# Kernel tuning notes

Hardware: AMD Instinct MI355X
Metric: run time of the kernel (lower is better)

## Reference

```python
import jax, jax.numpy as jnp
import numpy as np

N, E = 50000, 1600000
F_IN, C1, H, C2, G, NCLS = 256, 16, 4, 32, 64, 10


def setup_inputs() -> dict:
    ks = jax.random.split(jax.random.key(0), 14)
    x = jax.random.normal(ks[0], (N, F_IN), dtype=jnp.float32)
    edge_index = jax.random.randint(ks[1], (2, E), 0, N, dtype=jnp.int32)
    batch = jnp.sort(jax.random.randint(ks[2], (N,), 0, G, dtype=jnp.int32))
    s1 = 1.0 / np.sqrt(F_IN)
    s2 = 1.0 / np.sqrt(H * C1)
    s3 = 1.0 / np.sqrt(C2)
    return {
        "x": x,
        "edge_index": edge_index,
        "batch": batch,
        "W1": jax.random.normal(ks[3], (F_IN, H * C1), jnp.float32) * s1,
        "att_src1": jax.random.normal(ks[4], (H, C1), jnp.float32) * s2,
        "att_dst1": jax.random.normal(ks[5], (H, C1), jnp.float32) * s2,
        "b1": jnp.zeros((H * C1,), jnp.float32),
        "W2": jax.random.normal(ks[6], (H * C1, C2), jnp.float32) * s2,
        "att_src2": jax.random.normal(ks[7], (1, C2), jnp.float32) * s3,
        "att_dst2": jax.random.normal(ks[8], (1, C2), jnp.float32) * s3,
        "b2": jnp.zeros((C2,), jnp.float32),
        "fc_w": jax.random.normal(ks[9], (C2, NCLS), jnp.float32) * s3,
        "fc_b": jnp.zeros((NCLS,), jnp.float32),
    }


def _gat_conv(x, src, dst, W, a_src, a_dst, b, concat):
    # PyG GATConv: linear per head, LeakyReLU(0.2) edge scores,
    # softmax over incoming edges per destination node, weighted scatter-sum.
    n = x.shape[0]
    heads, ch = a_src.shape
    h = (x @ W).reshape(n, heads, ch)                       # [N, H, C]
    a_s = (h * a_src).sum(-1)                               # [N, H]
    a_d = (h * a_dst).sum(-1)                               # [N, H]
    e = jax.nn.leaky_relu(a_s[src] + a_d[dst], 0.2)         # [E', H]
    m = jax.ops.segment_max(e, dst, num_segments=n)         # [N, H]
    w = jnp.exp(e - m[dst])
    den = jax.ops.segment_sum(w, dst, num_segments=n)
    alpha = w / den[dst]                                    # [E', H]
    out = jax.ops.segment_sum(alpha[:, :, None] * h[src], dst, num_segments=n)
    out = out.reshape(n, heads * ch) if concat else out.mean(axis=1)
    return out + b


def reference(x, edge_index, batch, W1, att_src1, att_dst1, b1,
              W2, att_src2, att_dst2, b2, fc_w, fc_b):
    n = x.shape[0]
    loops = jnp.arange(n, dtype=edge_index.dtype)           # add_self_loops=True
    src = jnp.concatenate([edge_index[0], loops])
    dst = jnp.concatenate([edge_index[1], loops])

    h = jax.nn.elu(_gat_conv(x, src, dst, W1, att_src1, att_dst1, b1, True))
    h = jax.nn.elu(_gat_conv(h, src, dst, W2, att_src2, att_dst2, b2, False))

    # global mean pool over graphs
    sums = jax.ops.segment_sum(h, batch, num_segments=G)    # [G, C2]
    cnt = jax.ops.segment_sum(jnp.ones((n,), h.dtype), batch, num_segments=G)
    pooled = sums / jnp.maximum(cnt, 1.0)[:, None]

    logits = pooled @ fc_w + fc_b
    return jax.nn.log_softmax(logits, axis=1)
```

## Files before the change

### kernel.cpp

```cpp
#include <hip/hip_runtime.h>
#include <hip/hip_bf16.h>

#define GV 64
#define NCLSV 10
#define C2V 32

using short8 = __attribute__((ext_vector_type(8))) short;
using short4v = __attribute__((ext_vector_type(4))) short;
using f32x4 = __attribute__((ext_vector_type(4))) float;

__device__ __forceinline__ float lrelu(float v) { return v > 0.f ? v : 0.2f * v; }
__device__ __forceinline__ float eluf(float v) { return v > 0.f ? v : expf(v) - 1.f; }

__device__ __forceinline__ unsigned short fbf(float f) {
    unsigned u = __float_as_uint(f);
    u += 0x7fff + ((u >> 16) & 1);
    return (unsigned short)(u >> 16);
}
__device__ __forceinline__ float bff(unsigned short h) {
    return __uint_as_float((unsigned)h << 16);
}
__device__ __forceinline__ unsigned f2h(float f) {
    union { _Float16 h; unsigned short u; } cv;
    cv.h = (_Float16)f;
    return (unsigned)cv.u;
}
__device__ __forceinline__ float h2f(unsigned short u) {
    union { unsigned short u; _Float16 h; } cv;
    cv.u = u;
    return (float)cv.h;
}

__global__ void zero_kernel(int* p, int n) {
    int i = blockIdx.x * blockDim.x + threadIdx.x;
    if (i < n) p[i] = 0;
}

__global__ void wprep_kernel(const float* __restrict__ W1, const float* __restrict__ W2,
                             short* __restrict__ wt, short* __restrict__ wt2) {
    int t = blockIdx.x * blockDim.x + threadIdx.x;
    for (int e = t; e < 16384; e += gridDim.x * blockDim.x) {
        int k = e >> 6, ch = e & 63;
        wt[ch * 256 + k] = (short)fbf(W1[e]);
    }
    for (int e = t; e < 2048; e += gridDim.x * blockDim.x) {
        int k = e >> 5, ch = e & 31;
        wt2[ch * 64 + k] = (short)fbf(W2[e]);
    }
}

__global__ __launch_bounds__(256) void gemm1_mfma_kernel(
    const float* __restrict__ x, const short* __restrict__ wt,
    const float* __restrict__ as_w, const float* __restrict__ ad_w,
    unsigned short* __restrict__ h1b, float* __restrict__ as1, float* __restrict__ ad1, int N) {
    __shared__ __align__(16) short xs[32 * 256];
    int b0 = blockIdx.x * 32;
    int tid = threadIdx.x;
    #pragma unroll
    for (int i = 0; i < 8; ++i) {
        int e = (tid + i * 256) * 4;
        int node = e >> 8, k = e & 255;
        float4 v = make_float4(0.f, 0.f, 0.f, 0.f);
        if (b0 + node < N) v = *(const float4*)&x[(size_t)(b0 + node) * 256 + k];
        short4v hv;
        hv[0] = (short)fbf(v.x); hv[1] = (short)fbf(v.y);
        hv[2] = (short)fbf(v.z); hv[3] = (short)fbf(v.w);
        int bo = node * 512 + k * 2;
        int sw = bo ^ ((node & 7) << 4);
        *(short4v*)((char*)xs + sw) = hv;
    }
    __syncthreads();
    int w = tid >> 6, lane = tid & 63;
    int ng = w >> 1, cg = w & 1;
    int g = lane >> 4, q = lane & 15;
    int rowb = ng * 16 + q;
    int kb = g * 8;
    f32x4 acc[2];
    acc[0] = (f32x4){0.f, 0.f, 0.f, 0.f};
    acc[1] = (f32x4){0.f, 0.f, 0.f, 0.f};
    #pragma unroll
    for (int ks = 0; ks < 8; ++ks) {
        int kk = ks * 32 + kb;
        int off = (rowb * 512 + kk * 2) ^ ((rowb & 7) << 4);
        short8 a = *(const short8*)((const char*)xs + off);
        #pragma unroll
        for (int ct = 0; ct < 2; ++ct) {
            int ch = cg * 32 + ct * 16 + q;
            short8 b = *(const short8*)(wt + ch * 256 + kk);
            acc[ct] = __builtin_amdgcn_mfma_f32_16x16x32_bf16(a, b, acc[ct], 0, 0, 0);
        }
    }
    #pragma unroll
    for (int ct = 0; ct < 2; ++ct) {
        int chi = cg * 32 + ct * 16 + q;
        float asw = as_w[chi], adw = ad_w[chi];
        int head = cg * 2 + ct;
        #pragma unroll
        for (int r = 0; r < 4; ++r) {
            int node = b0 + ng * 16 + g * 4 + r;
            float val = acc[ct][r];
            if (node < N) h1b[(size_t)node * 64 + chi] = fbf(val);
            float vs = val * asw, vd = val * adw;
            vs += __shfl_xor(vs, 1); vs += __shfl_xor(vs, 2);
            vs += __shfl_xor(vs, 4); vs += __shfl_xor(vs, 8);
            vd += __shfl_xor(vd, 1); vd += __shfl_xor(vd, 2);
            vd += __shfl_xor(vd, 4); vd += __shfl_xor(vd, 8);
            if (q == 0 && node < N) {
                as1[node * 4 + head] = vs;
                ad1[node * 4 + head] = vd;
            }
        }
    }
}

__global__ __launch_bounds__(256) void bucketPre_kernel(
    const int* __restrict__ ei, int E, int EE, int* __restrict__ bcnt,
    int* __restrict__ pbase) {
    __shared__ int hist[256];
    int span = (EE + gridDim.x - 1) / gridDim.x;
    int s0 = blockIdx.x * span;
    int s1 = min(s0 + span, EE);
    hist[threadIdx.x] = 0;
    __syncthreads();
    for (int i = s0 + threadIdx.x; i < s1; i += 256) {
        int d = (i < E) ? ei[E + i] : i - E;
        atomicAdd(&hist[d >> 8], 1);
    }
    __syncthreads();
    int c = hist[threadIdx.x];
    int base = 0;
    if (c) base = atomicAdd(&bcnt[threadIdx.x], c);
    pbase[blockIdx.x * 256 + threadIdx.x] = base;
}

__global__ void bscan_kernel(const int* __restrict__ bcnt, int* __restrict__ bucketoff,
                             int* __restrict__ rowoff, int N, int EE) {
    __shared__ int wtot[4];
    int v = bcnt[threadIdx.x];
    int lane = threadIdx.x & 63, w = threadIdx.x >> 6;
    int inc = v;
    for (int o = 1; o < 64; o <<= 1) { int t = __shfl_up(inc, o); if (lane >= o) inc += t; }
    if (lane == 63) wtot[w] = inc;
    __syncthreads();
    int woff = 0;
    #pragma unroll
    for (int i = 0; i < 4; ++i) woff += (i < w) ? wtot[i] : 0;
    bucketoff[threadIdx.x + 1] = woff + inc;
    if (threadIdx.x == 0) { bucketoff[0] = 0; rowoff[N] = EE; }
}

__global__ __launch_bounds__(256) void bucketA_kernel(
    const int* __restrict__ ei, int E, int EE,
    const int* __restrict__ bucketoff, const int* __restrict__ pbase,
    int* __restrict__ bbuf) {
    __shared__ int base[256];
    __shared__ int cur[256];
    int span = (EE + gridDim.x - 1) / gridDim.x;
    int s0 = blockIdx.x * span;
    int s1 = min(s0 + span, EE);
    if (s0 >= s1) return;
    base[threadIdx.x] = bucketoff[threadIdx.x] + pbase[blockIdx.x * 256 + threadIdx.x];
    cur[threadIdx.x] = 0;
    __syncthreads();
    for (int i = s0 + threadIdx.x; i < s1; i += 256) {
        int s, d;
        if (i < E) { s = ei[i]; d = ei[E + i]; } else { s = d = i - E; }
        int b = d >> 8;
        int lr = atomicAdd(&cur[b], 1);
        bbuf[base[b] + lr] = ((d & 255) << 24) | s;
    }
}

__global__ __launch_bounds__(256) void bucketB_kernel(
    const int* __restrict__ bucketoff, const int* __restrict__ bbuf,
    const float* __restrict__ as1, const float* __restrict__ ad1,
    int* __restrict__ rowoff, int* __restrict__ ssrc, int4* __restrict__ wrec, int N) {
    int k = blockIdx.x;
    __shared__ int cnt[256];
    __shared__ int excl[256];
    __shared__ int cur[256];
    __shared__ int wtot[4];
    cnt[threadIdx.x] = 0; cur[threadIdx.x] = 0;
    __syncthreads();
    int lo = bucketoff[k], hi = bucketoff[k + 1];
    for (int i = lo + threadIdx.x; i < hi; i += 256)
        atomicAdd(&cnt[(bbuf[i] >> 24) & 255], 1);
    __syncthreads();
    int v = cnt[threadIdx.x];
    int lane = threadIdx.x & 63, w = threadIdx.x >> 6;
    int inc = v;
    for (int o = 1; o < 64; o <<= 1) { int t = __shfl_up(inc, o); if (lane >= o) inc += t; }
    if (lane == 63) wtot[w] = inc;
    __syncthreads();
    int woff = 0;
    #pragma unroll
    for (int i = 0; i < 4; ++i) woff += (i < w) ? wtot[i] : 0;
    int e = woff + inc - v;
    excl[threadIdx.x] = e;
    int dst = (k << 8) + threadIdx.x;
    if (dst < N) rowoff[dst] = lo + e;
    __syncthreads();
    int dbase = k << 8;
    for (int i = lo + threadIdx.x; i < hi; i += 256) {
        int pv = bbuf[i];
        int dlow = (pv >> 24) & 255;
        int s = pv & 0xFFFFFF;
        int d = dbase + dlow;
        int lr = atomicAdd(&cur[dlow], 1);
        int pos = lo + excl[dlow] + lr;
        ssrc[pos] = s;
        float4 a4 = *(const float4*)&as1[s * 4];
        float4 d4 = *(const float4*)&ad1[d * 4];
        float w0 = __expf(lrelu(a4.x + d4.x));
        float w1 = __expf(lrelu(a4.y + d4.y));
        float w2 = __expf(lrelu(a4.z + d4.z));
        float w3 = __expf(lrelu(a4.w + d4.w));
        int4 rec;
        rec.x = s;
        rec.y = (int)(f2h(w0) | (f2h(w1) << 16));
        rec.z = (int)(f2h(w2) | (f2h(w3) << 16));
        rec.w = 0;
        wrec[pos] = rec;
    }
}

__global__ __launch_bounds__(256) void gat1_kernel(
    const int* __restrict__ rowoff, const int4* __restrict__ wrec,
    const unsigned short* __restrict__ h1b, const float* __restrict__ b1,
    unsigned short* __restrict__ h2b, int N) {
    int wv = threadIdx.x >> 6;
    int lane = threadIdx.x & 63;
    int row = blockIdx.x * 4 + wv;
    if (row >= N) return;
    int beg = rowoff[row], end = rowoff[row + 1];
    int par = lane >> 3, co = lane & 7, hq = co >> 1;
    float den = 0.f;
    float a[8];
    #pragma unroll
    for (int i = 0; i < 8; ++i) a[i] = 0.f;
    for (int t = beg + par; t < end; t += 8) {
        int4 rec = wrec[t];
        unsigned wpair = (hq & 2) ? (unsigned)rec.z : (unsigned)rec.y;
        unsigned wb = (hq & 1) ? (wpair >> 16) : (wpair & 0xFFFFu);
        float w = h2f((unsigned short)wb);
        den += w;
        short8 p = *(const short8*)&h1b[(size_t)rec.x * 64 + 8 * co];
        a[0] += w * bff((unsigned short)p[0]);
        a[1] += w * bff((unsigned short)p[1]);
        a[2] += w * bff((unsigned short)p[2]);
        a[3] += w * bff((unsigned short)p[3]);
        a[4] += w * bff((unsigned short)p[4]);
        a[5] += w * bff((unsigned short)p[5]);
        a[6] += w * bff((unsigned short)p[6]);
        a[7] += w * bff((unsigned short)p[7]);
    }
    den += __shfl_xor(den, 8);
    den += __shfl_xor(den, 16);
    den += __shfl_xor(den, 32);
    #pragma unroll
    for (int i = 0; i < 8; ++i) {
        a[i] += __shfl_xor(a[i], 8);
        a[i] += __shfl_xor(a[i], 16);
        a[i] += __shfl_xor(a[i], 32);
    }
    if (par == 0) {
        float r = 1.f / den;
        short8 o;
        #pragma unroll
        for (int i = 0; i < 8; ++i)
            o[i] = (short)fbf(eluf(a[i] * r + b1[8 * co + i]));
        *(short8*)&h2b[(size_t)row * 64 + 8 * co] = o;
    }
}

__global__ __launch_bounds__(256) void gemm2_mfma_kernel(
    const unsigned short* __restrict__ h2b, const short* __restrict__ wt2,
    const float* __restrict__ as_w, const float* __restrict__ ad_w,
    unsigned short* __restrict__ t2b, float* __restrict__ as2, float* __restrict__ ad2, int N) {
    __shared__ __align__(16) short xs[64 * 64];
    int b0 = blockIdx.x * 64;
    int tid = threadIdx.x;
    #pragma unroll
    for (int i = 0; i < 2; ++i) {
        int e = (tid + i * 256) * 8;
        int node = e >> 6, k = e & 63;
        short8 v = (short8){0, 0, 0, 0, 0, 0, 0, 0};
        if (b0 + node < N) v = *(const short8*)&h2b[(size_t)(b0 + node) * 64 + k];
        int bo = node * 128 + k * 2;
        int sw = bo ^ ((node & 7) << 4);
        *(short8*)((char*)xs + sw) = v;
    }
    __syncthreads();
    int w = tid >> 6, lane = tid & 63;
    int g = lane >> 4, q = lane & 15;
    int rowb = w * 16 + q;
    int kb = g * 8;
    f32x4 acc[2];
    acc[0] = (f32x4){0.f, 0.f, 0.f, 0.f};
    acc[1] = (f32x4){0.f, 0.f, 0.f, 0.f};
    #pragma unroll
    for (int ks = 0; ks < 2; ++ks) {
        int kk = ks * 32 + kb;
        int off = (rowb * 128 + kk * 2) ^ ((rowb & 7) << 4);
        short8 a = *(const short8*)((const char*)xs + off);
        #pragma unroll
        for (int ct = 0; ct < 2; ++ct) {
            int ch = ct * 16 + q;
            short8 b = *(const short8*)(wt2 + ch * 64 + kk);
            acc[ct] = __builtin_amdgcn_mfma_f32_16x16x32_bf16(a, b, acc[ct], 0, 0, 0);
        }
    }
    float asw0 = as_w[q], adw0 = ad_w[q];
    float asw1 = as_w[16 + q], adw1 = ad_w[16 + q];
    #pragma unroll
    for (int r = 0; r < 4; ++r) {
        int node = b0 + w * 16 + g * 4 + r;
        float v0 = acc[0][r], v1 = acc[1][r];
        if (node < N) {
            t2b[(size_t)node * 32 + q] = fbf(v0);
            t2b[(size_t)node * 32 + 16 + q] = fbf(v1);
        }
        float vs = v0 * asw0 + v1 * asw1;
        float vd = v0 * adw0 + v1 * adw1;
        vs += __shfl_xor(vs, 1); vs += __shfl_xor(vs, 2);
        vs += __shfl_xor(vs, 4); vs += __shfl_xor(vs, 8);
        vd += __shfl_xor(vd, 1); vd += __shfl_xor(vd, 2);
        vd += __shfl_xor(vd, 4); vd += __shfl_xor(vd, 8);
        if (q == 0 && node < N) {
            as2[node] = vs;
            ad2[node] = vd;
        }
    }
}

__global__ __launch_bounds__(256) void gat2_kernel(
    const int* __restrict__ rowoff, const int* __restrict__ ssrc,
    const float* __restrict__ as2, const float* __restrict__ ad2,
    const unsigned short* __restrict__ t2b, const float* __restrict__ b2,
    float* __restrict__ h3, int N) {
    int wv = threadIdx.x >> 6;
    int lane = threadIdx.x & 63;
    int row = blockIdx.x * 4 + wv;
    if (row >= N) return;
    int beg = rowoff[row], end = rowoff[row + 1];
    int par = lane >> 2, co = lane & 3;
    float adv = ad2[row];
    float den = 0.f;
    float a[8];
    #pragma unroll
    for (int i = 0; i < 8; ++i) a[i] = 0.f;
    for (int t = beg + par; t < end; t += 16) {
        int s0 = ssrc[t];
        float w = __expf(lrelu(as2[s0] + adv));
        den += w;
        short8 p = *(const short8*)&t2b[(size_t)s0 * 32 + 8 * co];
        a[0] += w * bff((unsigned short)p[0]);
        a[1] += w * bff((unsigned short)p[1]);
        a[2] += w * bff((unsigned short)p[2]);
        a[3] += w * bff((unsigned short)p[3]);
        a[4] += w * bff((unsigned short)p[4]);
        a[5] += w * bff((unsigned short)p[5]);
        a[6] += w * bff((unsigned short)p[6]);
        a[7] += w * bff((unsigned short)p[7]);
    }
    den += __shfl_xor(den, 4);
    den += __shfl_xor(den, 8);
    den += __shfl_xor(den, 16);
    den += __shfl_xor(den, 32);
    #pragma unroll
    for (int i = 0; i < 8; ++i) {
        a[i] += __shfl_xor(a[i], 4);
        a[i] += __shfl_xor(a[i], 8);
        a[i] += __shfl_xor(a[i], 16);
        a[i] += __shfl_xor(a[i], 32);
    }
    if (par == 0) {
        float r = 1.f / den;
        float4 o0, o1;
        o0.x = eluf(a[0] * r + b2[8 * co]);
        o0.y = eluf(a[1] * r + b2[8 * co + 1]);
        o0.z = eluf(a[2] * r + b2[8 * co + 2]);
        o0.w = eluf(a[3] * r + b2[8 * co + 3]);
        o1.x = eluf(a[4] * r + b2[8 * co + 4]);
        o1.y = eluf(a[5] * r + b2[8 * co + 5]);
        o1.z = eluf(a[6] * r + b2[8 * co + 6]);
        o1.w = eluf(a[7] * r + b2[8 * co + 7]);
        *(float4*)&h3[(size_t)row * 32 + 8 * co] = o0;
        *(float4*)&h3[(size_t)row * 32 + 8 * co + 4] = o1;
    }
}

__device__ __forceinline__ int lowerb(const int* __restrict__ a, int n, int v) {
    int lo = 0, hi = n;
    while (lo < hi) {
        int mid = (lo + hi) >> 1;
        if (a[mid] < v) lo = mid + 1; else hi = mid;
    }
    return lo;
}

__global__ __launch_bounds__(256) void pool_kernel(
    const float* __restrict__ h3, const int* __restrict__ batch,
    float* __restrict__ pooled, float* __restrict__ cnt, int N) {
    int g = blockIdx.x;
    __shared__ int bounds[2];
    if (threadIdx.x == 0) bounds[0] = lowerb(batch, N, g);
    else if (threadIdx.x == 1) bounds[1] = lowerb(batch, N, g + 1);
    __syncthreads();
    int lo = bounds[0], hi = bounds[1];
    int c = threadIdx.x & 31;
    int grp = threadIdx.x >> 5;
    float s = 0.f;
    for (int n = lo + grp; n < hi; n += 8) s += h3[(size_t)n * 32 + c];
    __shared__ float red[8][33];
    red[grp][c] = s;
    __syncthreads();
    if (grp == 0) {
        float t = 0.f;
        for (int k = 0; k < 8; ++k) t += red[k][c];
        pooled[g * C2V + c] = t;
        if (c == 0) cnt[g] = (float)(hi - lo);
    }
}

__global__ void final_kernel(const float* __restrict__ pooled, const float* __restrict__ cnt,
                             const float* __restrict__ fc_w, const float* __restrict__ fc_b,
                             float* __restrict__ out) {
    int g = threadIdx.x;
    if (g >= GV) return;
    float c = cnt[g];
    c = c > 1.f ? c : 1.f;
    float p[C2V];
    for (int j = 0; j < C2V; ++j) p[j] = pooled[g * C2V + j] / c;
    float l[NCLSV];
    float mx = -1e30f;
    for (int k = 0; k < NCLSV; ++k) {
        float acc = fc_b[k];
        for (int j = 0; j < C2V; ++j) acc += p[j] * fc_w[j * NCLSV + k];
        l[k] = acc;
        mx = fmaxf(mx, acc);
    }
    float s = 0.f;
    for (int k = 0; k < NCLSV; ++k) s += expf(l[k] - mx);
    float lse = mx + logf(s);
    for (int k = 0; k < NCLSV; ++k) out[g * NCLSV + k] = l[k] - lse;
}

extern "C" void kernel_launch(void* const* d_in, const int* in_sizes, int n_in,
                              void* d_out, int out_size, void* d_ws, size_t ws_size,
                              hipStream_t stream) {
    const float* x = (const float*)d_in[0];
    const int* ei = (const int*)d_in[1];
    const int* batch = (const int*)d_in[2];
    const float* W1 = (const float*)d_in[3];
    const float* att_src1 = (const float*)d_in[4];
    const float* att_dst1 = (const float*)d_in[5];
    const float* b1 = (const float*)d_in[6];
    const float* W2 = (const float*)d_in[7];
    const float* att_src2 = (const float*)d_in[8];
    const float* att_dst2 = (const float*)d_in[9];
    const float* b2 = (const float*)d_in[10];
    const float* fc_w = (const float*)d_in[11];
    const float* fc_b = (const float*)d_in[12];
    float* out = (float*)d_out;

    int N = in_sizes[0] / 256;
    int E = in_sizes[1] / 2;
    int EE = E + N;
    int NB = (N + 255) >> 8;

    float* ws = (float*)d_ws;
    size_t off = 0;
    int* bcnt = (int*)(ws + off);      off += 256;
    size_t zTot = off;
    int* pbase = (int*)(ws + off);     off += 1024 * 256;
    int* bucketoff = (int*)(ws + off); off += 257;
    float* pooled = ws + off;          off += (size_t)GV * C2V;
    float* cnt = ws + off;             off += (size_t)GV;
    int* rowoff = (int*)(ws + off);    off += (size_t)N + 1;
    int* bbuf = (int*)(ws + off);      off += (size_t)EE;
    int* ssrc = (int*)(ws + off);      off += (size_t)EE;
    off = (off + 3) & ~(size_t)3;
    int4* wrec = (int4*)(ws + off);    off += (size_t)4 * EE;
    short* wt = (short*)(ws + off);    off += 8192;
    short* wt2 = (short*)(ws + off);   off += 1024;
    unsigned short* h1b = (unsigned short*)(ws + off); off += (size_t)32 * N;
    float* as1 = ws + off;             off += (size_t)4 * N;
    float* ad1 = ws + off;             off += (size_t)4 * N;
    unsigned short* h2b = (unsigned short*)(ws + off); off += (size_t)32 * N;
    unsigned short* t2b = (unsigned short*)(ws + off); off += (size_t)16 * N;
    float* as2 = ws + off;             off += (size_t)N;
    float* ad2 = ws + off;             off += (size_t)N;
    float* h3 = ws + off;              off += (size_t)32 * N;

    zero_kernel<<<1, 256, 0, stream>>>((int*)ws, (int)zTot);
    wprep_kernel<<<9, 256, 0, stream>>>(W1, W2, wt, wt2);

    gemm1_mfma_kernel<<<(N + 31) / 32, 256, 0, stream>>>(
        x, wt, att_src1, att_dst1, h1b, as1, ad1, N);

    bucketPre_kernel<<<1024, 256, 0, stream>>>(ei, E, EE, bcnt, pbase);
    bscan_kernel<<<1, 256, 0, stream>>>(bcnt, bucketoff, rowoff, N, EE);
    bucketA_kernel<<<1024, 256, 0, stream>>>(ei, E, EE, bucketoff, pbase, bbuf);
    bucketB_kernel<<<NB, 256, 0, stream>>>(bucketoff, bbuf, as1, ad1, rowoff, ssrc, wrec, N);

    gat1_kernel<<<(N + 3) / 4, 256, 0, stream>>>(rowoff, wrec, h1b, b1, h2b, N);

    gemm2_mfma_kernel<<<(N + 63) / 64, 256, 0, stream>>>(
        h2b, wt2, att_src2, att_dst2, t2b, as2, ad2, N);

    gat2_kernel<<<(N + 3) / 4, 256, 0, stream>>>(rowoff, ssrc, as2, ad2, t2b, b2, h3, N);

    pool_kernel<<<GV, 256, 0, stream>>>(h3, batch, pooled, cnt, N);
    final_kernel<<<1, 64, 0, stream>>>(pooled, cnt, fc_w, fc_b, out);
}
```

Before: 233.4 us.

## Split layer-1 features into head-pair halves and aggregate in two passes

Layer-1 node features are stored as two 32-channel tables, one per head pair, instead of one 64-channel table. The edge-weight computation moves out of bucketB into a new per-row edgew kernel that writes two 8-byte records per edge. gat1 then runs twice, once per half, with 16 edges in flight per wave. Each pass gathers from a table half the size, aiming for better cache hit rates on the random source gathers. The cost is an extra kernel launch, a second pass over rowoff and the edge records, and duplicated source indices in both record arrays.

New measurement: 249.8 us. 1.07x slower.

```diff
diff --git a/kernel.cpp b/kernel.cpp
--- a/kernel.cpp
+++ b/kernel.cpp
@@ -52,7 +52,8 @@
 __global__ __launch_bounds__(256) void gemm1_mfma_kernel(
     const float* __restrict__ x, const short* __restrict__ wt,
     const float* __restrict__ as_w, const float* __restrict__ ad_w,
-    unsigned short* __restrict__ h1b, float* __restrict__ as1, float* __restrict__ ad1, int N) {
+    unsigned short* __restrict__ h1lo, unsigned short* __restrict__ h1hi,
+    float* __restrict__ as1, float* __restrict__ ad1, int N) {
     __shared__ __align__(16) short xs[32 * 256];
     int b0 = blockIdx.x * 32;
     int tid = threadIdx.x;
@@ -90,16 +91,18 @@
             acc[ct] = __builtin_amdgcn_mfma_f32_16x16x32_bf16(a, b, acc[ct], 0, 0, 0);
         }
     }
+    unsigned short* dst = cg ? h1hi : h1lo;
     #pragma unroll
     for (int ct = 0; ct < 2; ++ct) {
         int chi = cg * 32 + ct * 16 + q;
+        int ch32 = ct * 16 + q;
         float asw = as_w[chi], adw = ad_w[chi];
         int head = cg * 2 + ct;
         #pragma unroll
         for (int r = 0; r < 4; ++r) {
             int node = b0 + ng * 16 + g * 4 + r;
             float val = acc[ct][r];
-            if (node < N) h1b[(size_t)node * 64 + chi] = fbf(val);
+            if (node < N) dst[(size_t)node * 32 + ch32] = fbf(val);
             float vs = val * asw, vd = val * adw;
             vs += __shfl_xor(vs, 1); vs += __shfl_xor(vs, 2);
             vs += __shfl_xor(vs, 4); vs += __shfl_xor(vs, 8);
@@ -173,8 +176,7 @@
 
 __global__ __launch_bounds__(256) void bucketB_kernel(
     const int* __restrict__ bucketoff, const int* __restrict__ bbuf,
-    const float* __restrict__ as1, const float* __restrict__ ad1,
-    int* __restrict__ rowoff, int* __restrict__ ssrc, int4* __restrict__ wrec, int N) {
+    int* __restrict__ rowoff, int* __restrict__ ssrc, int N) {
     int k = blockIdx.x;
     __shared__ int cnt[256];
     __shared__ int excl[256];
@@ -200,51 +202,56 @@
     int dst = (k << 8) + threadIdx.x;
     if (dst < N) rowoff[dst] = lo + e;
     __syncthreads();
-    int dbase = k << 8;
     for (int i = lo + threadIdx.x; i < hi; i += 256) {
         int pv = bbuf[i];
         int dlow = (pv >> 24) & 255;
-        int s = pv & 0xFFFFFF;
-        int d = dbase + dlow;
         int lr = atomicAdd(&cur[dlow], 1);
-        int pos = lo + excl[dlow] + lr;
-        ssrc[pos] = s;
-        float4 a4 = *(const float4*)&as1[s * 4];
-        float4 d4 = *(const float4*)&ad1[d * 4];
-        float w0 = __expf(lrelu(a4.x + d4.x));
-        float w1 = __expf(lrelu(a4.y + d4.y));
-        float w2 = __expf(lrelu(a4.z + d4.z));
-        float w3 = __expf(lrelu(a4.w + d4.w));
-        int4 rec;
-        rec.x = s;
-        rec.y = (int)(f2h(w0) | (f2h(w1) << 16));
-        rec.z = (int)(f2h(w2) | (f2h(w3) << 16));
-        rec.w = 0;
-        wrec[pos] = rec;
-    }
-}
-
-__global__ __launch_bounds__(256) void gat1_kernel(
-    const int* __restrict__ rowoff, const int4* __restrict__ wrec,
-    const unsigned short* __restrict__ h1b, const float* __restrict__ b1,
-    unsigned short* __restrict__ h2b, int N) {
+        ssrc[lo + excl[dlow] + lr] = pv & 0xFFFFFF;
+    }
+}
+
+__global__ __launch_bounds__(256) void edgew_kernel(
+    const int* __restrict__ rowoff, const int* __restrict__ ssrc,
+    const float* __restrict__ as1, const float* __restrict__ ad1,
+    int2* __restrict__ wrecA, int2* __restrict__ wrecB, int N) {
     int wv = threadIdx.x >> 6;
     int lane = threadIdx.x & 63;
     int row = blockIdx.x * 4 + wv;
     if (row >= N) return;
     int beg = rowoff[row], end = rowoff[row + 1];
-    int par = lane >> 3, co = lane & 7, hq = co >> 1;
+    float4 d4 = *(const float4*)&ad1[row * 4];
+    for (int t = beg + lane; t < end; t += 64) {
+        int s = ssrc[t];
+        float4 a4 = *(const float4*)&as1[s * 4];
+        float w0 = __expf(lrelu(a4.x + d4.x));
+        float w1 = __expf(lrelu(a4.y + d4.y));
+        float w2 = __expf(lrelu(a4.z + d4.z));
+        float w3 = __expf(lrelu(a4.w + d4.w));
+        wrecA[t] = make_int2(s, (int)(f2h(w0) | (f2h(w1) << 16)));
+        wrecB[t] = make_int2(s, (int)(f2h(w2) | (f2h(w3) << 16)));
+    }
+}
+
+__global__ __launch_bounds__(256) void gat1_kernel(
+    const int* __restrict__ rowoff, const int2* __restrict__ wrec,
+    const unsigned short* __restrict__ tab, const float* __restrict__ b1,
+    unsigned short* __restrict__ h2b, int N, int ho) {
+    int wv = threadIdx.x >> 6;
+    int lane = threadIdx.x & 63;
+    int row = blockIdx.x * 4 + wv;
+    if (row >= N) return;
+    int beg = rowoff[row], end = rowoff[row + 1];
+    int par = lane >> 2, co = lane & 3;
     float den = 0.f;
     float a[8];
     #pragma unroll
     for (int i = 0; i < 8; ++i) a[i] = 0.f;
-    for (int t = beg + par; t < end; t += 8) {
-        int4 rec = wrec[t];
-        unsigned wpair = (hq & 2) ? (unsigned)rec.z : (unsigned)rec.y;
-        unsigned wb = (hq & 1) ? (wpair >> 16) : (wpair & 0xFFFFu);
-        float w = h2f((unsigned short)wb);
+    for (int t = beg + par; t < end; t += 16) {
+        int2 rec = wrec[t];
+        unsigned wu = (unsigned)rec.y;
+        float w = h2f((unsigned short)((co & 2) ? (wu >> 16) : (wu & 0xFFFFu)));
         den += w;
-        short8 p = *(const short8*)&h1b[(size_t)rec.x * 64 + 8 * co];
+        short8 p = *(const short8*)&tab[(size_t)rec.x * 32 + 8 * co];
         a[0] += w * bff((unsigned short)p[0]);
         a[1] += w * bff((unsigned short)p[1]);
         a[2] += w * bff((unsigned short)p[2]);
@@ -254,22 +261,25 @@
         a[6] += w * bff((unsigned short)p[6]);
         a[7] += w * bff((unsigned short)p[7]);
     }
+    den += __shfl_xor(den, 4);
     den += __shfl_xor(den, 8);
     den += __shfl_xor(den, 16);
     den += __shfl_xor(den, 32);
     #pragma unroll
     for (int i = 0; i < 8; ++i) {
+        a[i] += __shfl_xor(a[i], 4);
         a[i] += __shfl_xor(a[i], 8);
         a[i] += __shfl_xor(a[i], 16);
         a[i] += __shfl_xor(a[i], 32);
     }
     if (par == 0) {
         float r = 1.f / den;
+        int cbase = (ho >> 1) * 32 + 8 * co;
         short8 o;
         #pragma unroll
         for (int i = 0; i < 8; ++i)
-            o[i] = (short)fbf(eluf(a[i] * r + b1[8 * co + i]));
-        *(short8*)&h2b[(size_t)row * 64 + 8 * co] = o;
+            o[i] = (short)fbf(eluf(a[i] * r + b1[cbase + i]));
+        *(short8*)&h2b[(size_t)row * 64 + cbase] = o;
     }
 }
 
@@ -475,36 +485,44 @@
     size_t zTot = off;
     int* pbase = (int*)(ws + off);     off += 1024 * 256;
     int* bucketoff = (int*)(ws + off); off += 257;
+    off = (off + 3) & ~(size_t)3;
     float* pooled = ws + off;          off += (size_t)GV * C2V;
     float* cnt = ws + off;             off += (size_t)GV;
     int* rowoff = (int*)(ws + off);    off += (size_t)N + 1;
+    off = (off + 3) & ~(size_t)3;
     int* bbuf = (int*)(ws + off);      off += (size_t)EE;
     int* ssrc = (int*)(ws + off);      off += (size_t)EE;
     off = (off + 3) & ~(size_t)3;
-    int4* wrec = (int4*)(ws + off);    off += (size_t)4 * EE;
+    int2* wrecA = (int2*)(ws + off);   off += (size_t)2 * EE;
+    int2* wrecB = (int2*)(ws + off);   off += (size_t)2 * EE;
     short* wt = (short*)(ws + off);    off += 8192;
     short* wt2 = (short*)(ws + off);   off += 1024;
-    unsigned short* h1b = (unsigned short*)(ws + off); off += (size_t)32 * N;
+    unsigned short* h1lo = (unsigned short*)(ws + off); off += (size_t)16 * N;
+    unsigned short* h1hi = (unsigned short*)(ws + off); off += (size_t)16 * N;
     float* as1 = ws + off;             off += (size_t)4 * N;
     float* ad1 = ws + off;             off += (size_t)4 * N;
     unsigned short* h2b = (unsigned short*)(ws + off); off += (size_t)32 * N;
     unsigned short* t2b = (unsigned short*)(ws + off); off += (size_t)16 * N;
     float* as2 = ws + off;             off += (size_t)N;
     float* ad2 = ws + off;             off += (size_t)N;
+    off = (off + 3) & ~(size_t)3;
     float* h3 = ws + off;              off += (size_t)32 * N;
 
     zero_kernel<<<1, 256, 0, stream>>>((int*)ws, (int)zTot);
     wprep_kernel<<<9, 256, 0, stream>>>(W1, W2, wt, wt2);
 
     gemm1_mfma_kernel<<<(N + 31) / 32, 256, 0, stream>>>(
-        x, wt, att_src1, att_dst1, h1b, as1, ad1, N);
+        x, wt, att_src1, att_dst1, h1lo, h1hi, as1, ad1, N);
 
     bucketPre_kernel<<<1024, 256, 0, stream>>>(ei, E, EE, bcnt, pbase);
     bscan_kernel<<<1, 256, 0, stream>>>(bcnt, bucketoff, rowoff, N, EE);
     bucketA_kernel<<<1024, 256, 0, stream>>>(ei, E, EE, bucketoff, pbase, bbuf);
-    bucketB_kernel<<<NB, 256, 0, stream>>>(bucketoff, bbuf, as1, ad1, rowoff, ssrc, wrec, N);
-
-    gat1_kernel<<<(N + 3) / 4, 256, 0, stream>>>(rowoff, wrec, h1b, b1, h2b, N);
+    bucketB_kernel<<<NB, 256, 0, stream>>>(bucketoff, bbuf, rowoff, ssrc, N);
+
+    edgew_kernel<<<(N + 3) / 4, 256, 0, stream>>>(rowoff, ssrc, as1, ad1, wrecA, wrecB, N);
+
+    gat1_kernel<<<(N + 3) / 4, 256, 0, stream>>>(rowoff, wrecA, h1lo, b1, h2b, N, 0);
+    gat1_kernel<<<(N + 3) / 4, 256, 0, stream>>>(rowoff, wrecB, h1hi, b1, h2b, N, 2);
 
     gemm2_mfma_kernel<<<(N + 63) / 64, 256, 0, stream>>>(
         h2b, wt2, att_src2, att_dst2, t2b, as2, ad2, N);
```
